# Kernel tuning notes

Hardware: AMD Instinct MI355X
Metric: run time of the kernel (lower is better)

## Reference

```python
import jax, jax.numpy as jnp
import numpy as np

EPS = 1e-5

def _layer_norm(y, w, b):
    mu = y.mean(-1, keepdims=True)
    var = jnp.mean((y - mu) ** 2, axis=-1, keepdims=True)
    return (y - mu) * jax.lax.rsqrt(var + EPS) * w + b


def setup_inputs() -> dict:
    key = jax.random.key(0)
    ks = jax.random.split(key, 8)
    B, D, H, W = 1, 96, 96, 96
    N, R, K = 16, 6, 4
    x = jax.random.normal(ks[0], (B, D, H, W), jnp.float32)
    x_proj_weight = jax.random.normal(ks[1], (K, R + 2 * N, D), jnp.float32) * 0.05
    dt_projs_weight = jax.random.normal(ks[2], (K, D, R), jnp.float32) * 0.1
    dt_projs_bias = jax.random.normal(ks[3], (K, D), jnp.float32) * 0.1
    A_logs = jax.random.normal(ks[4], (K * D, N), jnp.float32)
    Ds = jax.random.normal(ks[5], (K * D,), jnp.float32) * 0.1
    ln_w = jnp.ones((D,), jnp.float32)
    ln_b = jnp.zeros((D,), jnp.float32)
    return {"x": x, "x_proj_weight": x_proj_weight, "dt_projs_weight": dt_projs_weight,
            "dt_projs_bias": dt_projs_bias, "A_logs": A_logs, "Ds": Ds,
            "ln_w": ln_w, "ln_b": ln_b}


def reference(x, x_proj_weight, dt_projs_weight, dt_projs_bias, A_logs, Ds, ln_w, ln_b):
    B, D, H, W = x.shape
    L = H * W
    K = x_proj_weight.shape[0]            # 4 scan directions
    N = A_logs.shape[1]                   # d_state
    R = dt_projs_weight.shape[2]          # dt_rank

    # ---- CrossScan: 4 directional flattenings -> xs [B, K, D, L]
    xs0 = x.reshape(B, D, L)
    xs1 = jnp.swapaxes(x, 2, 3).reshape(B, D, L)
    xs = jnp.stack([xs0, xs1, xs0[:, :, ::-1], xs1[:, :, ::-1]], axis=1)

    # ---- input-dependent projections
    x_dbl = jnp.einsum('bkdl,kcd->bkcl', xs, x_proj_weight)    # [B,K,R+2N,L]
    dts = x_dbl[:, :, :R]
    Bs = x_dbl[:, :, R:R + N]                                  # [B,K,N,L]
    Cs = x_dbl[:, :, R + N:]                                   # [B,K,N,L]
    dts = jnp.einsum('bkrl,kdr->bkdl', dts, dt_projs_weight)   # [B,K,D,L]

    # ---- selective scan (S6), delta_softplus=True, fp32
    delta = jax.nn.softplus(dts + dt_projs_bias[None, :, :, None])   # [B,K,D,L]
    A = -jnp.exp(A_logs).reshape(K, D, N)                             # [K,D,N]
    dA = jnp.exp(jnp.einsum('bkdl,kdn->bkdln', delta, A))             # [B,K,D,L,N]
    dBu = jnp.einsum('bkdl,bknl,bkdl->bkdln', delta, Bs, xs)          # delta*B*u

    def combine(c1, c2):
        a1, b1 = c1
        a2, b2 = c2
        return a1 * a2, a2 * b1 + b2

    _, h = jax.lax.associative_scan(combine, (dA, dBu), axis=3)       # h_t over L

    y = jnp.einsum('bkdln,bknl->bkdl', h, Cs)
    y = y + xs * Ds.reshape(K, D)[None, :, :, None]                   # [B,K,D,L]

    # ---- CrossMerge: undo the 4 directional scans and sum
    ys = y[:, 0:2] + y[:, 2:4, :, ::-1]                               # [B,2,D,L]
    ym = ys[:, 0] + jnp.swapaxes(ys[:, 1].reshape(B, D, W, H), 2, 3).reshape(B, D, L)

    # ---- out_norm (LayerNorm over D) and reshape to [B,H,W,D]
    yout = jnp.swapaxes(ym, 1, 2)                                     # [B,L,D]
    yout = _layer_norm(yout, ln_w, ln_b).reshape(B, H, W, D)
    return yout.astype(x.dtype)
```

## Files before the change

kernel.cpp:

```cpp
#include <hip/hip_runtime.h>
#include <math.h>

constexpr int cD = 96, cL = 9216, cK = 4;
constexpr int CL = 36, NCH = 256;
constexpr long cDL = (long)cD * cL;
constexpr float LOG2E = 1.44269504088896f;

constexpr long OFF_XT    = 0;
constexpr long OFF_DELTA = OFF_XT    + cDL;
constexpr long OFF_BC    = OFF_DELTA + 4L*cDL;
constexpr long OFF_Y     = OFF_BC    + 4L*cL*32;
constexpr long OFF_PG    = OFF_Y     + 4L*cDL;
constexpr long OFF_SG    = OFF_PG    + 384L*256*16;

__device__ __forceinline__ float4 a2prep(float4 v) {
    return make_float4(-LOG2E * exp2f(LOG2E * v.x), -LOG2E * exp2f(LOG2E * v.y),
                       -LOG2E * exp2f(LOG2E * v.z), -LOG2E * exp2f(LOG2E * v.w));
}
template<int C>
__device__ __forceinline__ float qperm(float v) {
    return __int_as_float(__builtin_amdgcn_mov_dpp(__float_as_int(v), C, 0xf, 0xf, true));
}

__global__ __launch_bounds__(256) void kT(const float* __restrict__ x,
                                          float* __restrict__ xT) {
    __shared__ float t[32][33];
    const int h0 = blockIdx.x * 32, w0 = blockIdx.y * 32, d = blockIdx.z;
    const float* xd = x + (long)d * cL;
    float* xtd = xT + (long)d * cL;
    for (int o = threadIdx.x; o < 1024; o += 256) {
        int i = o >> 5, j = o & 31;
        t[i][j] = xd[(h0 + i) * 96 + w0 + j];
    }
    __syncthreads();
    for (int o = threadIdx.x; o < 1024; o += 256) {
        int i = o >> 5, j = o & 31;
        xtd[(w0 + i) * 96 + h0 + j] = t[j][i];
    }
}

__global__ __launch_bounds__(256) void kA(const float* __restrict__ x,
                                          const float* __restrict__ xT,
                                          const float* __restrict__ xpw,
                                          const float* __restrict__ dtw,
                                          const float* __restrict__ dtb,
                                          float* __restrict__ delta,
                                          float* __restrict__ BC) {
    __shared__ float xs[96][64];
    __shared__ float xdbl[38][65];
    __shared__ float dtw_l[96 * 6];
    __shared__ float dtb_l[96];
    const int p0 = blockIdx.x * 64;
    const int k  = blockIdx.y;
    const int tid = threadIdx.x;
    const float* src = (k & 1) ? xT : x;

    for (int o = tid; o < 96 * 64; o += 256) {
        int dd = o >> 6, pp = o & 63;
        xs[dd][pp] = src[(long)dd * cL + p0 + pp];
    }
    for (int o = tid; o < 96 * 6; o += 256) dtw_l[o] = dtw[k * 96 * 6 + o];
    if (tid < 96) dtb_l[tid] = dtb[k * 96 + tid];
    __syncthreads();

    const int lane = tid & 63;
    const int c0 = __builtin_amdgcn_readfirstlane((tid >> 6) * 10);
    const float* wk = xpw + (long)k * 38 * 96;
    float acc[10];
    #pragma unroll
    for (int i = 0; i < 10; ++i) acc[i] = 0.f;
    #pragma unroll 4
    for (int dd = 0; dd < 96; ++dd) {
        float xv = xs[dd][lane];
        #pragma unroll
        for (int i = 0; i < 10; ++i) {
            int c = c0 + i; c = c > 37 ? 37 : c;
            acc[i] = fmaf(xv, wk[c * 96 + dd], acc[i]);
        }
    }
    #pragma unroll
    for (int i = 0; i < 10; ++i) {
        int c = c0 + i; c = c > 37 ? 37 : c;
        xdbl[c][lane] = acc[i];
    }
    __syncthreads();

    for (int o = tid; o < 64 * 16; o += 256) {
        int n = o & 15, pp = o >> 4;
        int P = p0 + pp;
        int q = (k < 2) ? P : (9215 - P);
        int ch = q / 36, j = q - ch * 36;
        long idx = (((long)k * 36 + j) * 256 + ch) * 32 + n;
        BC[idx]      = xdbl[6 + n][pp];
        BC[idx + 16] = xdbl[22 + n][pp];
    }
    for (int o = tid; o < 96 * 64; o += 256) {
        int dd = o >> 6, pp = o & 63;
        float s = dtb_l[dd];
        #pragma unroll
        for (int r = 0; r < 6; ++r) s = fmaf(xdbl[r][pp], dtw_l[dd * 6 + r], s);
        float sp = fmaxf(s, 0.f) + __logf(1.f + __expf(-fabsf(s)));
        delta[((long)(k * 96 + dd)) * cL + p0 + pp] = sp;
    }
}

__global__ __launch_bounds__(512, 5) void kS1(const float* __restrict__ x,
                                              const float* __restrict__ xT,
                                              const float* __restrict__ delta,
                                              const float* __restrict__ BC,
                                              const float* __restrict__ Alog,
                                              float* __restrict__ Pg,
                                              float* __restrict__ Sg) {
    const int tid = threadIdx.x;
    const int n0 = (tid & 3) * 4, chl = tid >> 2;
    const int hb = blockIdx.x & 1, seq = blockIdx.x >> 1;
    const int k = seq / 96, d = seq % 96, rev = k >> 1;
    const int ch = hb * 128 + chl;
    const int q0 = ch * CL;

    const float4 a2 = a2prep(*(const float4*)(Alog + (long)seq * 16 + n0));
    const float* dRow = delta + (long)seq * cL;
    const float* xRow = ((k & 1) ? xT : x) + (long)d * cL;
    const float* bc = BC + ((long)k * 36 * 256 + ch) * 32 + n0;

    float4 h = make_float4(0.f, 0.f, 0.f, 0.f);
    float sdl = 0.f;
#define STEP1(DL, XV, B) { \
        float t = (DL) * (XV); sdl += (DL); \
        h.x = fmaf(exp2f((DL)*a2.x), h.x, t*(B).x); \
        h.y = fmaf(exp2f((DL)*a2.y), h.y, t*(B).y); \
        h.z = fmaf(exp2f((DL)*a2.z), h.z, t*(B).z); \
        h.w = fmaf(exp2f((DL)*a2.w), h.w, t*(B).w); }
    #pragma unroll
    for (int g = 0; g < 9; ++g) {
        const float* bj = bc + (long)(4 * g) * 8192;
        float4 B0 = *(const float4*)(bj);
        float4 B1 = *(const float4*)(bj + 8192);
        float4 B2 = *(const float4*)(bj + 16384);
        float4 B3 = *(const float4*)(bj + 24576);
        float4 d4, x4;
        if (!rev) {
            d4 = *(const float4*)(dRow + q0 + 4 * g);
            x4 = *(const float4*)(xRow + q0 + 4 * g);
            STEP1(d4.x, x4.x, B0) STEP1(d4.y, x4.y, B1)
            STEP1(d4.z, x4.z, B2) STEP1(d4.w, x4.w, B3)
        } else {
            d4 = *(const float4*)(dRow + 9212 - q0 - 4 * g);
            x4 = *(const float4*)(xRow + 9212 - q0 - 4 * g);
            STEP1(d4.w, x4.w, B0) STEP1(d4.z, x4.z, B1)
            STEP1(d4.y, x4.y, B2) STEP1(d4.x, x4.x, B3)
        }
    }
#undef STEP1
    long o = ((long)seq * NCH + ch) * 16 + n0;
    *(float4*)(Pg + o) = make_float4(exp2f(a2.x*sdl), exp2f(a2.y*sdl),
                                     exp2f(a2.z*sdl), exp2f(a2.w*sdl));
    *(float4*)(Sg + o) = h;
}

__global__ __launch_bounds__(512, 3) void kS2(const float* __restrict__ x,
                                              const float* __restrict__ xT,
                                              const float* __restrict__ delta,
                                              const float* __restrict__ BC,
                                              const float* __restrict__ Alog,
                                              const float* __restrict__ Dsv,
                                              const float* __restrict__ Pg,
                                              const float* __restrict__ Sg,
                                              float* __restrict__ y) {
    __shared__ float lp[NCH][16];
    __shared__ float ls[NCH][16];
    __shared__ float ybuf[4608 + 48];
    float* gpf = &lp[0][0];
    const int tid = threadIdx.x;
    const int hb = blockIdx.x & 1, seq = blockIdx.x >> 1;
    const int k = seq / 96, d = seq % 96, rev = k >> 1;

    #pragma unroll
    for (int i = 0; i < 8; ++i) {
        ((float*)lp)[tid + i * 512] = Pg[(long)seq * 4096 + tid + i * 512];
        ((float*)ls)[tid + i * 512] = Sg[(long)seq * 4096 + tid + i * 512];
    }
    __syncthreads();

    const int sn = tid & 15, sg = tid >> 4;
    float LPe[8], LSe[8];
    {
        float P = 1.f, S = 0.f;
        #pragma unroll
        for (int i = 0; i < 8; ++i) {
            LPe[i] = P; LSe[i] = S;
            float p = lp[sg * 8 + i][sn], s = ls[sg * 8 + i][sn];
            S = fmaf(p, S, s); P = p * P;
        }
        __syncthreads();
        gpf[tid] = P; gpf[512 + tid] = S;
    }
    __syncthreads();
    #pragma unroll
    for (int off = 1; off < 32; off <<= 1) {
        float pc = gpf[tid], sc = gpf[512 + tid];
        float pn = pc, snn = sc;
        if (sg >= off) {
            pn  = pc * gpf[tid - off * 16];
            snn = fmaf(pc, gpf[512 + tid - off * 16], sc);
        }
        __syncthreads();
        gpf[tid] = pn; gpf[512 + tid] = snn;
        __syncthreads();
    }
    const float GS = (sg == 0) ? 0.f : gpf[512 + tid - 16];
    #pragma unroll
    for (int i = 0; i < 8; ++i) ls[sg * 8 + i][sn] = fmaf(LPe[i], GS, LSe[i]);
    __syncthreads();

    const int n0 = (tid & 3) * 4, chl = tid >> 2;
    const int r = tid & 3;
    const int ch = hb * 128 + chl;
    const int q0 = ch * CL;
    const int slB = chl * CL;
    const float4 a2 = a2prep(*(const float4*)(Alog + (long)seq * 16 + n0));
    const float Dv = Dsv[seq];
    const float* dRow = delta + (long)seq * cL;
    const float* xRow = ((k & 1) ? xT : x) + (long)d * cL;
    const float* bc = BC + ((long)k * 36 * 256 + ch) * 32 + n0;
    float4 h = *(float4*)&ls[ch][n0];
    float yhold = 0.f;

#define STEP2(DL, XV, B, C, SI) { \
        float t = (DL) * (XV); \
        h.x = fmaf(exp2f((DL)*a2.x), h.x, t*(B).x); \
        h.y = fmaf(exp2f((DL)*a2.y), h.y, t*(B).y); \
        h.z = fmaf(exp2f((DL)*a2.z), h.z, t*(B).z); \
        h.w = fmaf(exp2f((DL)*a2.w), h.w, t*(B).w); \
        float pv = fmaf(h.x, (C).x, fmaf(h.y, (C).y, fmaf(h.z, (C).z, h.w * (C).w))); \
        pv += qperm<0xB1>(pv); \
        pv += qperm<0x4E>(pv); \
        if ((SI) == r) yhold = fmaf(Dv, (XV), pv); }
    #pragma unroll
    for (int g = 0; g < 9; ++g) {
        const float* bj = bc + (long)(4 * g) * 8192;
        float4 B0 = *(const float4*)(bj);
        float4 C0 = *(const float4*)(bj + 16);
        float4 B1 = *(const float4*)(bj + 8192);
        float4 C1 = *(const float4*)(bj + 8192 + 16);
        float4 B2 = *(const float4*)(bj + 16384);
        float4 C2 = *(const float4*)(bj + 16384 + 16);
        float4 B3 = *(const float4*)(bj + 24576);
        float4 C3 = *(const float4*)(bj + 24576 + 16);
        float4 d4, x4;
        if (!rev) {
            d4 = *(const float4*)(dRow + q0 + 4 * g);
            x4 = *(const float4*)(xRow + q0 + 4 * g);
            STEP2(d4.x, x4.x, B0, C0, 0) STEP2(d4.y, x4.y, B1, C1, 1)
            STEP2(d4.z, x4.z, B2, C2, 2) STEP2(d4.w, x4.w, B3, C3, 3)
        } else {
            d4 = *(const float4*)(dRow + 9212 - q0 - 4 * g);
            x4 = *(const float4*)(xRow + 9212 - q0 - 4 * g);
            STEP2(d4.w, x4.w, B0, C0, 0) STEP2(d4.z, x4.z, B1, C1, 1)
            STEP2(d4.y, x4.y, B2, C2, 2) STEP2(d4.x, x4.x, B3, C3, 3)
        }
        int sl = slB + 4 * g + r;
        int yloc = rev ? 4607 - sl : sl;
        ybuf[yloc + yloc / 96] = yhold;
    }
#undef STEP2
    __syncthreads();

    const int sb = rev ? (1 - hb) * 4608 : hb * 4608;
    float* yrow = y + (long)seq * cL;
    if (k & 1) {
        const int w0 = sb / 96;
        for (int o = tid; o < 4608; o += 512) {
            int hh = o / 48, wl = o - hh * 48;
            yrow[hh * 96 + w0 + wl] = ybuf[wl * 97 + hh];
        }
    } else {
        for (int o = tid; o < 4608; o += 512) {
            yrow[sb + o] = ybuf[o + o / 96];
        }
    }
}

__global__ __launch_bounds__(256) void kE(const float* __restrict__ y,
                                          const float* __restrict__ lnw,
                                          const float* __restrict__ lnb,
                                          float* __restrict__ out) {
    __shared__ float vs[96][36];
    __shared__ float red[8][32], red2[8][32];
    __shared__ float MU[32], RS[32];
    const int tid = threadIdx.x;
    const int p0 = blockIdx.x * 32;

    for (int o = tid; o < 96 * 8; o += 256) {
        int dd = o >> 3, j = o & 7;
        const float* r0 = y + (long)dd * cL + p0;
        const float* r1 = y + cDL + (long)dd * cL + p0;
        const float* r2 = y + 2 * cDL + (long)dd * cL + p0;
        const float* r3 = y + 3 * cDL + (long)dd * cL + p0;
        float4 a = ((const float4*)r0)[j];
        float4 b = ((const float4*)r1)[j];
        float4 c = ((const float4*)r2)[j];
        float4 e = ((const float4*)r3)[j];
        *(float4*)&vs[dd][4 * j] = make_float4(a.x + b.x + c.x + e.x,
                                               a.y + b.y + c.y + e.y,
                                               a.z + b.z + c.z + e.z,
                                               a.w + b.w + c.w + e.w);
    }
    __syncthreads();

    const int p = tid & 31, part = tid >> 5;
    float s = 0.f, s2 = 0.f;
    for (int dd = part * 12; dd < part * 12 + 12; ++dd) {
        float v = vs[dd][p];
        s += v; s2 = fmaf(v, v, s2);
    }
    red[part][p] = s; red2[part][p] = s2;
    __syncthreads();
    if (tid < 32) {
        float S = 0.f, S2 = 0.f;
        #pragma unroll
        for (int q = 0; q < 8; ++q) { S += red[q][tid]; S2 += red2[q][tid]; }
        float m = S * (1.f / 96.f);
        MU[tid] = m;
        RS[tid] = rsqrtf(S2 * (1.f / 96.f) - m * m + 1e-5f);
    }
    __syncthreads();
    for (int o = tid; o < 32 * 96; o += 256) {
        int pl = o / 96, dd = o - pl * 96;
        out[(long)(p0 + pl) * 96 + dd] = (vs[dd][pl] - MU[pl]) * RS[pl] * lnw[dd] + lnb[dd];
    }
}

extern "C" void kernel_launch(void* const* d_in, const int* in_sizes, int n_in,
                              void* d_out, int out_size, void* d_ws, size_t ws_size,
                              hipStream_t stream) {
    const float* x    = (const float*)d_in[0];
    const float* xpw  = (const float*)d_in[1];
    const float* dtw  = (const float*)d_in[2];
    const float* dtb  = (const float*)d_in[3];
    const float* Alog = (const float*)d_in[4];
    const float* Dsv  = (const float*)d_in[5];
    const float* lnw  = (const float*)d_in[6];
    const float* lnb  = (const float*)d_in[7];
    float* ws = (float*)d_ws;

    float* xT    = ws + OFF_XT;
    float* delta = ws + OFF_DELTA;
    float* BC    = ws + OFF_BC;
    float* y     = ws + OFF_Y;
    float* Pg    = ws + OFF_PG;
    float* Sg    = ws + OFF_SG;
    float* out   = (float*)d_out;

    kT<<<dim3(3, 3, 96), 256, 0, stream>>>(x, xT);
    kA<<<dim3(144, 4), 256, 0, stream>>>(x, xT, xpw, dtw, dtb, delta, BC);
    kS1<<<768, 512, 0, stream>>>(x, xT, delta, BC, Alog, Pg, Sg);
    kS2<<<768, 512, 0, stream>>>(x, xT, delta, BC, Alog, Dsv, Pg, Sg, y);
    kE<<<288, 256, 0, stream>>>(y, lnw, lnb, out);
}
```

Before: 97.43 us.

## Split chunk-carry scan into separate kernel and stage delta/x rows in LDS

The inter-chunk prefix combine moves out of the second scan kernel into a new small kernel kC, which writes per-chunk carry-in states back into Pg. The replay kernel kR then uses 256-thread blocks over quarter sequences, giving 1536 blocks with higher occupancy and no serial prefix phase. Both scan kernels now stage their contiguous delta and x segments in shared memory with coalesced float4 loads instead of strided per-thread global reads. The cost is one extra kernel launch and an extra global round trip for the carry states.

```diff
diff --git a/kernel.cpp b/kernel.cpp
--- a/kernel.cpp
+++ b/kernel.cpp
@@ -104,25 +104,32 @@
     }
 }
 
-__global__ __launch_bounds__(512, 5) void kS1(const float* __restrict__ x,
+__global__ __launch_bounds__(512, 6) void kS1(const float* __restrict__ x,
                                               const float* __restrict__ xT,
                                               const float* __restrict__ delta,
                                               const float* __restrict__ BC,
                                               const float* __restrict__ Alog,
                                               float* __restrict__ Pg,
                                               float* __restrict__ Sg) {
+    __shared__ float dls[4608], xls[4608];
     const int tid = threadIdx.x;
     const int n0 = (tid & 3) * 4, chl = tid >> 2;
     const int hb = blockIdx.x & 1, seq = blockIdx.x >> 1;
     const int k = seq / 96, d = seq % 96, rev = k >> 1;
     const int ch = hb * 128 + chl;
-    const int q0 = ch * CL;
-
-    const float4 a2 = a2prep(*(const float4*)(Alog + (long)seq * 16 + n0));
+
     const float* dRow = delta + (long)seq * cL;
     const float* xRow = ((k & 1) ? xT : x) + (long)d * cL;
+    const int sb2 = rev ? (1 - hb) * 4608 : hb * 4608;
+    for (int o = tid; o < 1152; o += 512) {
+        ((float4*)dls)[o] = ((const float4*)(dRow + sb2))[o];
+        ((float4*)xls)[o] = ((const float4*)(xRow + sb2))[o];
+    }
+    const float4 a2 = a2prep(*(const float4*)(Alog + (long)seq * 16 + n0));
     const float* bc = BC + ((long)k * 36 * 256 + ch) * 32 + n0;
-
+    __syncthreads();
+
+    const int sbase = chl * 36;
     float4 h = make_float4(0.f, 0.f, 0.f, 0.f);
     float sdl = 0.f;
 #define STEP1(DL, XV, B) { \
@@ -140,13 +147,13 @@
         float4 B3 = *(const float4*)(bj + 24576);
         float4 d4, x4;
         if (!rev) {
-            d4 = *(const float4*)(dRow + q0 + 4 * g);
-            x4 = *(const float4*)(xRow + q0 + 4 * g);
+            d4 = *(const float4*)(dls + sbase + 4 * g);
+            x4 = *(const float4*)(xls + sbase + 4 * g);
             STEP1(d4.x, x4.x, B0) STEP1(d4.y, x4.y, B1)
             STEP1(d4.z, x4.z, B2) STEP1(d4.w, x4.w, B3)
         } else {
-            d4 = *(const float4*)(dRow + 9212 - q0 - 4 * g);
-            x4 = *(const float4*)(xRow + 9212 - q0 - 4 * g);
+            d4 = *(const float4*)(dls + 4604 - sbase - 4 * g);
+            x4 = *(const float4*)(xls + 4604 - sbase - 4 * g);
             STEP1(d4.w, x4.w, B0) STEP1(d4.z, x4.z, B1)
             STEP1(d4.y, x4.y, B2) STEP1(d4.x, x4.x, B3)
         }
@@ -158,74 +165,73 @@
     *(float4*)(Sg + o) = h;
 }
 
-__global__ __launch_bounds__(512, 3) void kS2(const float* __restrict__ x,
-                                              const float* __restrict__ xT,
-                                              const float* __restrict__ delta,
-                                              const float* __restrict__ BC,
-                                              const float* __restrict__ Alog,
-                                              const float* __restrict__ Dsv,
-                                              const float* __restrict__ Pg,
-                                              const float* __restrict__ Sg,
-                                              float* __restrict__ y) {
-    __shared__ float lp[NCH][16];
-    __shared__ float ls[NCH][16];
-    __shared__ float ybuf[4608 + 48];
-    float* gpf = &lp[0][0];
-    const int tid = threadIdx.x;
-    const int hb = blockIdx.x & 1, seq = blockIdx.x >> 1;
+__global__ __launch_bounds__(256) void kC(float* __restrict__ Pg,
+                                          const float* __restrict__ Sg) {
+    __shared__ float gp[256], gs[256];
+    const int seq = blockIdx.x;
+    const int tid = threadIdx.x;
+    const int sn = tid & 15, sg = tid >> 4;
+    const long base = (long)seq * 4096 + sg * 256 + sn;
+
+    float LPe[16], LSe[16];
+    float P = 1.f, S = 0.f;
+    #pragma unroll
+    for (int i = 0; i < 16; ++i) {
+        float p = Pg[base + i * 16], s = Sg[base + i * 16];
+        LPe[i] = P; LSe[i] = S;
+        S = fmaf(p, S, s); P *= p;
+    }
+    gp[tid] = P; gs[tid] = S;
+    __syncthreads();
+    #pragma unroll
+    for (int off = 1; off < 16; off <<= 1) {
+        float pc = gp[tid], sc = gs[tid];
+        float pn = pc, s2 = sc;
+        if (sg >= off) {
+            pn = pc * gp[tid - off * 16];
+            s2 = fmaf(pc, gs[tid - off * 16], sc);
+        }
+        __syncthreads();
+        gp[tid] = pn; gs[tid] = s2;
+        __syncthreads();
+    }
+    const float GS = (sg == 0) ? 0.f : gs[tid - 16];
+    #pragma unroll
+    for (int i = 0; i < 16; ++i)
+        Pg[base + i * 16] = fmaf(LPe[i], GS, LSe[i]);
+}
+
+__global__ __launch_bounds__(256, 5) void kR(const float* __restrict__ x,
+                                             const float* __restrict__ xT,
+                                             const float* __restrict__ delta,
+                                             const float* __restrict__ BC,
+                                             const float* __restrict__ Alog,
+                                             const float* __restrict__ Dsv,
+                                             const float* __restrict__ hin,
+                                             float* __restrict__ y) {
+    __shared__ float dls[2304], xls[2304];
+    __shared__ float ybuf[2304 + 24];
+    const int tid = threadIdx.x;
+    const int n0 = (tid & 3) * 4, chl = tid >> 2, r = tid & 3;
+    const int qb = blockIdx.x & 3, seq = blockIdx.x >> 2;
     const int k = seq / 96, d = seq % 96, rev = k >> 1;
-
-    #pragma unroll
-    for (int i = 0; i < 8; ++i) {
-        ((float*)lp)[tid + i * 512] = Pg[(long)seq * 4096 + tid + i * 512];
-        ((float*)ls)[tid + i * 512] = Sg[(long)seq * 4096 + tid + i * 512];
-    }
-    __syncthreads();
-
-    const int sn = tid & 15, sg = tid >> 4;
-    float LPe[8], LSe[8];
-    {
-        float P = 1.f, S = 0.f;
-        #pragma unroll
-        for (int i = 0; i < 8; ++i) {
-            LPe[i] = P; LSe[i] = S;
-            float p = lp[sg * 8 + i][sn], s = ls[sg * 8 + i][sn];
-            S = fmaf(p, S, s); P = p * P;
-        }
-        __syncthreads();
-        gpf[tid] = P; gpf[512 + tid] = S;
-    }
-    __syncthreads();
-    #pragma unroll
-    for (int off = 1; off < 32; off <<= 1) {
-        float pc = gpf[tid], sc = gpf[512 + tid];
-        float pn = pc, snn = sc;
-        if (sg >= off) {
-            pn  = pc * gpf[tid - off * 16];
-            snn = fmaf(pc, gpf[512 + tid - off * 16], sc);
-        }
-        __syncthreads();
-        gpf[tid] = pn; gpf[512 + tid] = snn;
-        __syncthreads();
-    }
-    const float GS = (sg == 0) ? 0.f : gpf[512 + tid - 16];
-    #pragma unroll
-    for (int i = 0; i < 8; ++i) ls[sg * 8 + i][sn] = fmaf(LPe[i], GS, LSe[i]);
-    __syncthreads();
-
-    const int n0 = (tid & 3) * 4, chl = tid >> 2;
-    const int r = tid & 3;
-    const int ch = hb * 128 + chl;
-    const int q0 = ch * CL;
-    const int slB = chl * CL;
+    const int ch = qb * 64 + chl;
+
+    const float* dRow = delta + (long)seq * cL;
+    const float* xRow = ((k & 1) ? xT : x) + (long)d * cL;
+    const int sb = rev ? (3 - qb) * 2304 : qb * 2304;
+    for (int o = tid; o < 576; o += 256) {
+        ((float4*)dls)[o] = ((const float4*)(dRow + sb))[o];
+        ((float4*)xls)[o] = ((const float4*)(xRow + sb))[o];
+    }
     const float4 a2 = a2prep(*(const float4*)(Alog + (long)seq * 16 + n0));
     const float Dv = Dsv[seq];
-    const float* dRow = delta + (long)seq * cL;
-    const float* xRow = ((k & 1) ? xT : x) + (long)d * cL;
     const float* bc = BC + ((long)k * 36 * 256 + ch) * 32 + n0;
-    float4 h = *(float4*)&ls[ch][n0];
+    float4 h = *(const float4*)(hin + ((long)seq * NCH + ch) * 16 + n0);
+    __syncthreads();
+
+    const int sbase = chl * 36;
     float yhold = 0.f;
-
 #define STEP2(DL, XV, B, C, SI) { \
         float t = (DL) * (XV); \
         h.x = fmaf(exp2f((DL)*a2.x), h.x, t*(B).x); \
@@ -249,33 +255,32 @@
         float4 C3 = *(const float4*)(bj + 24576 + 16);
         float4 d4, x4;
         if (!rev) {
-            d4 = *(const float4*)(dRow + q0 + 4 * g);
-            x4 = *(const float4*)(xRow + q0 + 4 * g);
+            d4 = *(const float4*)(dls + sbase + 4 * g);
+            x4 = *(const float4*)(xls + sbase + 4 * g);
             STEP2(d4.x, x4.x, B0, C0, 0) STEP2(d4.y, x4.y, B1, C1, 1)
             STEP2(d4.z, x4.z, B2, C2, 2) STEP2(d4.w, x4.w, B3, C3, 3)
         } else {
-            d4 = *(const float4*)(dRow + 9212 - q0 - 4 * g);
-            x4 = *(const float4*)(xRow + 9212 - q0 - 4 * g);
+            d4 = *(const float4*)(dls + 2300 - sbase - 4 * g);
+            x4 = *(const float4*)(xls + 2300 - sbase - 4 * g);
             STEP2(d4.w, x4.w, B0, C0, 0) STEP2(d4.z, x4.z, B1, C1, 1)
             STEP2(d4.y, x4.y, B2, C2, 2) STEP2(d4.x, x4.x, B3, C3, 3)
         }
-        int sl = slB + 4 * g + r;
-        int yloc = rev ? 4607 - sl : sl;
+        int sl = sbase + 4 * g + r;
+        int yloc = rev ? 2303 - sl : sl;
         ybuf[yloc + yloc / 96] = yhold;
     }
 #undef STEP2
     __syncthreads();
 
-    const int sb = rev ? (1 - hb) * 4608 : hb * 4608;
     float* yrow = y + (long)seq * cL;
     if (k & 1) {
         const int w0 = sb / 96;
-        for (int o = tid; o < 4608; o += 512) {
-            int hh = o / 48, wl = o - hh * 48;
+        for (int o = tid; o < 2304; o += 256) {
+            int hh = o / 24, wl = o - hh * 24;
             yrow[hh * 96 + w0 + wl] = ybuf[wl * 97 + hh];
         }
     } else {
-        for (int o = tid; o < 4608; o += 512) {
+        for (int o = tid; o < 2304; o += 256) {
             yrow[sb + o] = ybuf[o + o / 96];
         }
     }
@@ -355,6 +360,7 @@
     kT<<<dim3(3, 3, 96), 256, 0, stream>>>(x, xT);
     kA<<<dim3(144, 4), 256, 0, stream>>>(x, xT, xpw, dtw, dtb, delta, BC);
     kS1<<<768, 512, 0, stream>>>(x, xT, delta, BC, Alog, Pg, Sg);
-    kS2<<<768, 512, 0, stream>>>(x, xT, delta, BC, Alog, Dsv, Pg, Sg, y);
+    kC<<<384, 256, 0, stream>>>(Pg, Sg);
+    kR<<<1536, 256, 0, stream>>>(x, xT, delta, BC, Alog, Dsv, Pg, y);
     kE<<<288, 256, 0, stream>>>(y, lnw, lnb, out);
 }
```

Result: faster. 92.09 us (median of 2 runs) (-5.5%).
